# Performance work log

Measured on AMD Instinct MI355X. Metric: run time of the kernel, lower is better.

## Reference

```python
import jax, jax.numpy as jnp
from jax import lax
import numpy as np

NPOINT = 2  # hardcoded in the original forward
INIT_DIST = 10000000000.0


def farthest_point_sample(xyz, npoint):
    # xyz: [B, N, 3] -> centroids: [B, npoint] int64
    B, N, _ = xyz.shape
    farthest0 = jnp.argmax(xyz[:, :, 1], axis=1)          # [B], max over y-coordinate
    distance0 = jnp.full((B, N), INIT_DIST, dtype=xyz.dtype)

    def step(carry, _):
        distance, farthest = carry
        centroid = jnp.take_along_axis(xyz, farthest[:, None, None], axis=1)  # [B,1,3]
        dist = jnp.sum((xyz - centroid) ** 2, axis=-1)     # [B,N]
        distance = jnp.minimum(distance, dist)             # where(dist<distance, dist, distance)
        new_farthest = jnp.argmax(distance, axis=-1)       # [B]
        return (distance, new_farthest), farthest          # record index BEFORE update (matches torch loop)

    (_, _), centroids = lax.scan(step, (distance0, farthest0), None, length=npoint)
    return centroids.T.astype(jnp.int64)                   # [B, npoint]


def setup_inputs() -> dict:
    key = jax.random.key(0)
    xyz = jax.random.normal(key, (1, 64, 3, 262144), dtype=jnp.float32)
    return {"xyz": xyz}


def reference(xyz):
    # forward: [1, B, 3, N] -> permute(0,1,3,2) -> [1, B, N, 3] -> squeeze(0) -> [B, N, 3]
    pts = jnp.transpose(xyz, (0, 1, 3, 2))[0]
    return farthest_point_sample(pts, NPOINT)
```

## Files before the change

### kernel.cpp

```cpp
#include <hip/hip_runtime.h>
#include <stdint.h>

static constexpr int NPTS  = 262144;
static constexpr int BATCH = 64;
static constexpr int BLKS1 = 32;
static constexpr int BLKS2 = 32;


__device__ __forceinline__ uint32_t map_f32(float f) {
    uint32_t u = __float_as_uint(f);
    return (u & 0x80000000u) ? ~u : (u | 0x80000000u);
}

__device__ __forceinline__ uint64_t pack_key(uint32_t vbits, int i) {
    return ((uint64_t)vbits << 32) | (uint32_t)(~i);
}

__device__ __forceinline__ uint64_t umax64(uint64_t a, uint64_t b) {
    return a > b ? a : b;
}

__device__ __forceinline__ uint64_t block_max_256(uint64_t k) {
    for (int off = 32; off > 0; off >>= 1)
        k = umax64(k, (uint64_t)__shfl_down((unsigned long long)k, off));
    __shared__ uint64_t s[4];
    int wid  = threadIdx.x >> 6;
    int lane = threadIdx.x & 63;
    if (lane == 0) s[wid] = k;
    __syncthreads();
    if (threadIdx.x == 0)
        for (int w = 1; w < 4; ++w) k = umax64(k, s[w]);
    return k;
}

__global__ __launch_bounds__(256) void k_argmax_y(const float* __restrict__ xyz,
                                                  uint64_t* __restrict__ part) {
    int b   = blockIdx.x / BLKS1;
    int blk = blockIdx.x % BLKS1;
    const int chunk = NPTS / BLKS1;
    const float4* Y4 = (const float4*)(xyz + (size_t)b * 3 * NPTS + NPTS
                                       + (size_t)blk * chunk);
    int base = blk * chunk;
    uint64_t bk = 0;
#pragma unroll 4
    for (int j = threadIdx.x; j < chunk / 4; j += 256) {
        float4 y = Y4[j];
        int i0 = base + j * 4;
        bk = umax64(bk, pack_key(map_f32(y.x), i0));
        bk = umax64(bk, pack_key(map_f32(y.y), i0 + 1));
        bk = umax64(bk, pack_key(map_f32(y.z), i0 + 2));
        bk = umax64(bk, pack_key(map_f32(y.w), i0 + 3));
    }
    bk = block_max_256(bk);
    if (threadIdx.x == 0) part[blockIdx.x] = bk;
}

__global__ __launch_bounds__(64) void k_final_f0(const float* __restrict__ xyz,
                                                 const uint64_t* __restrict__ part,
                                                 int* __restrict__ out,
                                                 float* __restrict__ cent) {
    int b = blockIdx.x;
    int t = threadIdx.x;
    uint64_t k = (t < BLKS1) ? part[b * BLKS1 + t] : 0;
    for (int off = 32; off > 0; off >>= 1)
        k = umax64(k, (uint64_t)__shfl_down((unsigned long long)k, off));
    if (t == 0) {
        int bi = (int)(~(uint32_t)k);
        out[b * 2 + 0] = bi;
        const float* base = xyz + (size_t)b * 3 * NPTS;
        cent[b * 3 + 0] = base[bi];
        cent[b * 3 + 1] = base[NPTS + bi];
        cent[b * 3 + 2] = base[2 * NPTS + bi];
    }
}

__global__ __launch_bounds__(256) void k_dist_argmax(const float* __restrict__ xyz,
                                                     const float* __restrict__ cent,
                                                     uint64_t* __restrict__ part) {
#pragma clang fp contract(off)
    int b   = blockIdx.x / BLKS2;
    int blk = blockIdx.x % BLKS2;
    const int chunk = NPTS / BLKS2;
    const float* base = xyz + (size_t)b * 3 * NPTS + (size_t)blk * chunk;
    const float4* X4 = (const float4*)base;
    const float4* Y4 = (const float4*)(base + NPTS);
    const float4* Z4 = (const float4*)(base + 2 * NPTS);
    float cx = cent[b * 3 + 0];
    float cy = cent[b * 3 + 1];
    float cz = cent[b * 3 + 2];
    int ib = blk * chunk;
    uint64_t bk = 0;
#pragma unroll 4
    for (int j = threadIdx.x; j < chunk / 4; j += 256) {
        float4 x = X4[j], y = Y4[j], z = Z4[j];
        int i0 = ib + j * 4;
        {
            float dx = x.x - cx, dy = y.x - cy, dz = z.x - cz;
            float d = (dx * dx + dy * dy) + dz * dz;
            bk = umax64(bk, pack_key(__float_as_uint(d), i0));
        }
        {
            float dx = x.y - cx, dy = y.y - cy, dz = z.y - cz;
            float d = (dx * dx + dy * dy) + dz * dz;
            bk = umax64(bk, pack_key(__float_as_uint(d), i0 + 1));
        }
        {
            float dx = x.z - cx, dy = y.z - cy, dz = z.z - cz;
            float d = (dx * dx + dy * dy) + dz * dz;
            bk = umax64(bk, pack_key(__float_as_uint(d), i0 + 2));
        }
        {
            float dx = x.w - cx, dy = y.w - cy, dz = z.w - cz;
            float d = (dx * dx + dy * dy) + dz * dz;
            bk = umax64(bk, pack_key(__float_as_uint(d), i0 + 3));
        }
    }
    bk = block_max_256(bk);
    if (threadIdx.x == 0) part[blockIdx.x] = bk;
}

__global__ __launch_bounds__(64) void k_final_f1(const uint64_t* __restrict__ part,
                                                 int* __restrict__ out) {
    int b = blockIdx.x;
    int t = threadIdx.x;
    uint64_t k = (t < BLKS2) ? part[b * BLKS2 + t] : 0;
    for (int off = 32; off > 0; off >>= 1)
        k = umax64(k, (uint64_t)__shfl_down((unsigned long long)k, off));
    if (t == 0) out[b * 2 + 1] = (int)(~(uint32_t)k);
}

extern "C" void kernel_launch(void* const* d_in, const int* in_sizes, int n_in,
                              void* d_out, int out_size, void* d_ws, size_t ws_size,
                              hipStream_t stream) {
    const float* xyz = (const float*)d_in[0];
    int* out = (int*)d_out;
    char* ws = (char*)d_ws;
    uint64_t* part1 = (uint64_t*)ws;
    float*    cent  = (float*)(ws + 16384);
    uint64_t* part2 = (uint64_t*)(ws + 17408);

    k_argmax_y   <<<BATCH * BLKS1, 256, 0, stream>>>(xyz, part1);
    k_final_f0   <<<BATCH,         64,  0, stream>>>(xyz, part1, out, cent);
    k_dist_argmax<<<BATCH * BLKS2, 256, 0, stream>>>(xyz, cent, part2);
    k_final_f1   <<<BATCH,         64,  0, stream>>>(part2, out);
}
```

Before: 274.9 us.

## Replace per-batch final reduction kernels with atomicMax and last-block completion

```diff
diff --git a/kernel.cpp b/kernel.cpp
--- a/kernel.cpp
+++ b/kernel.cpp
@@ -33,8 +33,8 @@
     return k;
 }
 
-__global__ __launch_bounds__(256) void k_argmax_y(const float* __restrict__ xyz,
-                                                  uint64_t* __restrict__ part) {
+__global__ __launch_bounds__(256) void k_pass1(const float* __restrict__ xyz,
+                                               uint64_t* __restrict__ key0) {
     int b   = blockIdx.x / BLKS1;
     int blk = blockIdx.x % BLKS1;
     const int chunk = NPTS / BLKS1;
@@ -52,42 +52,32 @@
         bk = umax64(bk, pack_key(map_f32(y.w), i0 + 3));
     }
     bk = block_max_256(bk);
-    if (threadIdx.x == 0) part[blockIdx.x] = bk;
+    if (threadIdx.x == 0)
+        atomicMax((unsigned long long*)&key0[b], (unsigned long long)bk);
 }
 
-__global__ __launch_bounds__(64) void k_final_f0(const float* __restrict__ xyz,
-                                                 const uint64_t* __restrict__ part,
-                                                 int* __restrict__ out,
-                                                 float* __restrict__ cent) {
-    int b = blockIdx.x;
-    int t = threadIdx.x;
-    uint64_t k = (t < BLKS1) ? part[b * BLKS1 + t] : 0;
-    for (int off = 32; off > 0; off >>= 1)
-        k = umax64(k, (uint64_t)__shfl_down((unsigned long long)k, off));
-    if (t == 0) {
-        int bi = (int)(~(uint32_t)k);
-        out[b * 2 + 0] = bi;
-        const float* base = xyz + (size_t)b * 3 * NPTS;
-        cent[b * 3 + 0] = base[bi];
-        cent[b * 3 + 1] = base[NPTS + bi];
-        cent[b * 3 + 2] = base[2 * NPTS + bi];
-    }
-}
-
-__global__ __launch_bounds__(256) void k_dist_argmax(const float* __restrict__ xyz,
-                                                     const float* __restrict__ cent,
-                                                     uint64_t* __restrict__ part) {
+__global__ __launch_bounds__(256) void k_pass2(const float* __restrict__ xyz,
+                                               const uint64_t* __restrict__ key0,
+                                               uint64_t* __restrict__ key1,
+                                               uint32_t* __restrict__ cnt,
+                                               int* __restrict__ out) {
 #pragma clang fp contract(off)
     int b   = blockIdx.x / BLKS2;
     int blk = blockIdx.x % BLKS2;
     const int chunk = NPTS / BLKS2;
-    const float* base = xyz + (size_t)b * 3 * NPTS + (size_t)blk * chunk;
+    const float* bbase = xyz + (size_t)b * 3 * NPTS;
+
+    uint64_t k0 = key0[b];
+    int if0 = (int)(~(uint32_t)k0);
+    float cx = bbase[if0];
+    float cy = bbase[NPTS + if0];
+    float cz = bbase[2 * NPTS + if0];
+    if (blk == 0 && threadIdx.x == 0) out[b * 2 + 0] = if0;
+
+    const float* base = bbase + (size_t)blk * chunk;
     const float4* X4 = (const float4*)base;
     const float4* Y4 = (const float4*)(base + NPTS);
     const float4* Z4 = (const float4*)(base + 2 * NPTS);
-    float cx = cent[b * 3 + 0];
-    float cy = cent[b * 3 + 1];
-    float cz = cent[b * 3 + 2];
     int ib = blk * chunk;
     uint64_t bk = 0;
 #pragma unroll 4
@@ -116,17 +106,15 @@
         }
     }
     bk = block_max_256(bk);
-    if (threadIdx.x == 0) part[blockIdx.x] = bk;
-}
-
-__global__ __launch_bounds__(64) void k_final_f1(const uint64_t* __restrict__ part,
-                                                 int* __restrict__ out) {
-    int b = blockIdx.x;
-    int t = threadIdx.x;
-    uint64_t k = (t < BLKS2) ? part[b * BLKS2 + t] : 0;
-    for (int off = 32; off > 0; off >>= 1)
-        k = umax64(k, (uint64_t)__shfl_down((unsigned long long)k, off));
-    if (t == 0) out[b * 2 + 1] = (int)(~(uint32_t)k);
+    if (threadIdx.x == 0) {
+        atomicMax((unsigned long long*)&key1[b], (unsigned long long)bk);
+        __threadfence();
+        uint32_t t = atomicAdd(&cnt[b], 1u);
+        if (t == BLKS2 - 1) {
+            uint64_t k1 = (uint64_t)atomicMax((unsigned long long*)&key1[b], 0ull);
+            out[b * 2 + 1] = (int)(~(uint32_t)k1);
+        }
+    }
 }
 
 extern "C" void kernel_launch(void* const* d_in, const int* in_sizes, int n_in,
@@ -135,12 +123,11 @@
     const float* xyz = (const float*)d_in[0];
     int* out = (int*)d_out;
     char* ws = (char*)d_ws;
-    uint64_t* part1 = (uint64_t*)ws;
-    float*    cent  = (float*)(ws + 16384);
-    uint64_t* part2 = (uint64_t*)(ws + 17408);
+    uint64_t* key0 = (uint64_t*)ws;
+    uint64_t* key1 = (uint64_t*)(ws + 512);
+    uint32_t* cnt  = (uint32_t*)(ws + 1024);
 
-    k_argmax_y   <<<BATCH * BLKS1, 256, 0, stream>>>(xyz, part1);
-    k_final_f0   <<<BATCH,         64,  0, stream>>>(xyz, part1, out, cent);
-    k_dist_argmax<<<BATCH * BLKS2, 256, 0, stream>>>(xyz, cent, part2);
-    k_final_f1   <<<BATCH,         64,  0, stream>>>(part2, out);
+    hipMemsetAsync(ws, 0, 2048, stream);
+    k_pass1<<<BATCH * BLKS1, 256, 0, stream>>>(xyz, key0);
+    k_pass2<<<BATCH * BLKS2, 256, 0, stream>>>(xyz, key0, key1, cnt, out);
 }
```

Result: slower. 375.3 us (+36.5%).
